# Optimization experiments

Measured on AMD Instinct MI355X. Metric: run time of the kernel, lower is better.

## Reference

```python
import jax, jax.numpy as jnp
import numpy as np

MIN_D, MAX_D = 0.1, 1.0
KSIZE = 5


def gaussian_kernel(ksize):
    sigma = ksize / 6.0
    x = jnp.arange(ksize, dtype=jnp.float32) - ksize // 2
    k1 = jnp.exp(-0.5 * x ** 2 / sigma ** 2)
    k1 = k1 / k1.sum()
    return (k1[:, None] * k1[None, :])[None, None]  # [1,1,k,k]


def setup_inputs() -> dict:
    key = jax.random.key(0)
    k1, k2 = jax.random.split(key)
    B, H, W = 8, 512, 512
    TH = TW = 512
    contrast_map = jax.random.normal(k1, (B, 1, H, W), dtype=jnp.float32)
    # uniform [0,1) randoms replacing the per-sample torch.rand calls
    rand_offsets = jax.random.uniform(k2, (B, TH, TW, 4, 2), dtype=jnp.float32)
    return {
        "contrast_map": contrast_map,
        "rand_offsets": rand_offsets,
        "smoothing_kernel": gaussian_kernel(KSIZE),
        "target_height": TH,
        "target_width": TW,
    }


def reference(contrast_map, rand_offsets, smoothing_kernel, target_height, target_width):
    B, _, H, W = contrast_map.shape
    # per-sample min-max normalization to [0,1]
    mn = contrast_map.min(axis=(1, 2, 3), keepdims=True)
    mx = contrast_map.max(axis=(1, 2, 3), keepdims=True)
    norm = jnp.where(mx > mn, (contrast_map - mn) / (mx - mn), jnp.zeros_like(contrast_map))
    # gaussian smoothing, same padding
    pad = KSIZE // 2
    smoothed = jax.lax.conv_general_dilated(
        norm, smoothing_kernel, window_strides=(1, 1),
        padding=[(pad, pad), (pad, pad)],
        dimension_numbers=("NCHW", "OIHW", "NCHW"))
    # contrast -> density: min_d + (max_d-min_d) * sqrt(c)
    density = MIN_D + (MAX_D - MIN_D) * jnp.sqrt(smoothed)  # [B,1,H,W]

    # nearest-index lookup:  h_idx = floor(i*H/TH) clamped
    hi = jnp.minimum((jnp.arange(target_height) * H) // target_height, H - 1)
    wi = jnp.minimum((jnp.arange(target_width) * W) // target_width, W - 1)
    local = density[:, 0][:, hi][:, :, wi]  # [B,TH,TW]

    # per-pixel sample count: >0.7 -> 4, >0.4 -> 2, else 1
    num_samples = jnp.where(local > 0.7, 4, jnp.where(local > 0.4, 2, 1))  # int [B,TH,TW]

    yb = jnp.linspace(-1.0, 1.0, target_height)
    xb = jnp.linspace(-1.0, 1.0, target_width)
    base = jnp.stack(jnp.broadcast_arrays(yb[:, None], xb[None, :]), axis=-1)  # [TH,TW,2] (y,x)
    cell = jnp.array([2.0 / target_height, 2.0 / target_width], dtype=jnp.float32)
    off = (rand_offsets - 0.5) * cell * 0.8  # [B,TH,TW,4,2]
    use_off = (num_samples > 1)[..., None, None]  # single-sample pixels use the base coord
    coords = base[None, :, :, None, :] + jnp.where(use_off, off, 0.0)  # [B,TH,TW,4,2]

    slot = jnp.arange(4)
    valid = slot[None, None, None, :] < num_samples[..., None]  # [B,TH,TW,4]
    weights = jnp.where(valid, local[..., None] / num_samples[..., None], 0.0)  # [B,TH,TW,4]
    return coords, weights, density
```

## Files before the change

kernel.cpp:

```cpp
#include <hip/hip_runtime.h>

static constexpr int B = 8, Himg = 512, Wimg = 512, TH = 512, TW = 512;
static constexpr int NPIX = B * Himg * Wimg;
static constexpr int BPB = 32;

typedef float f4 __attribute__((ext_vector_type(4)));
typedef float f2 __attribute__((ext_vector_type(2)));

__global__ __launch_bounds__(256) void minmax_kernel(const float* __restrict__ cm,
                                                     float* __restrict__ wsmin,
                                                     float* __restrict__ wsmax) {
    int b   = blockIdx.x / BPB;
    int blk = blockIdx.x % BPB;
    const f4* p = (const f4*)(cm + (size_t)b * Himg * Wimg);
    float mn = 3.4e38f, mx = -3.4e38f;
    int base = blk * 2048;
    #pragma unroll
    for (int k = 0; k < 8; ++k) {
        f4 v = p[base + k * 256 + threadIdx.x];
        mn = fminf(mn, fminf(fminf(v.x, v.y), fminf(v.z, v.w)));
        mx = fmaxf(mx, fmaxf(fmaxf(v.x, v.y), fmaxf(v.z, v.w)));
    }
    #pragma unroll
    for (int off = 32; off; off >>= 1) {
        mn = fminf(mn, __shfl_xor(mn, off));
        mx = fmaxf(mx, __shfl_xor(mx, off));
    }
    __shared__ float smn[4], smx[4];
    int wave = threadIdx.x >> 6, lane = threadIdx.x & 63;
    if (lane == 0) { smn[wave] = mn; smx[wave] = mx; }
    __syncthreads();
    if (threadIdx.x == 0) {
        mn = fminf(fminf(smn[0], smn[1]), fminf(smn[2], smn[3]));
        mx = fmaxf(fmaxf(smx[0], smx[1]), fmaxf(smx[2], smx[3]));
        wsmin[b * BPB + blk] = mn;
        wsmax[b * BPB + blk] = mx;
    }
}

__global__ __launch_bounds__(256) void density_kernel(const float* __restrict__ cm,
                                                      const float* __restrict__ kern,
                                                      const float* __restrict__ wsmin,
                                                      const float* __restrict__ wsmax,
                                                      float* __restrict__ dens) {
    __shared__ double tile[36][37];
    __shared__ double kd[25];
    int tid = threadIdx.x;
    int b = blockIdx.z;
    int bx = blockIdx.x * 32, by = blockIdx.y * 32;
    if (tid < 25) kd[tid] = (double)kern[tid];

    float mnf = 3.4e38f, mxf = -3.4e38f;
    #pragma unroll
    for (int k = 0; k < BPB; ++k) {
        mnf = fminf(mnf, wsmin[b * BPB + k]);
        mxf = fmaxf(mxf, wsmax[b * BPB + k]);
    }
    bool ok = mxf > mnf;
    double mn = (double)mnf;
    double inv = ok ? (1.0 / ((double)mxf - mn)) : 0.0;

    const float* img = cm + (size_t)b * Himg * Wimg;
    for (int idx = tid; idx < 36 * 36; idx += 256) {
        int r = idx / 36, c = idx % 36;
        int gy = by + r - 2, gx = bx + c - 2;
        double v = 0.0;
        if (gy >= 0 && gy < Himg && gx >= 0 && gx < Wimg) {
            double x = (double)img[gy * Wimg + gx];
            v = (x - mn) * inv;
        }
        tile[r][c] = v;
    }
    __syncthreads();

    for (int p = tid; p < 32 * 32; p += 256) {
        int oy = p >> 5, ox = p & 31;
        double s = 0.0;
        #pragma unroll
        for (int dy = 0; dy < 5; ++dy)
            #pragma unroll
            for (int dx = 0; dx < 5; ++dx)
                s += tile[oy + dy][ox + dx] * kd[dy * 5 + dx];
        double D = 0.1 + 0.9 * sqrt(s);
        int code = D > 0.7 ? 2 : (D > 0.4 ? 1 : 0);

        unsigned u = __float_as_uint((float)D);
        u = (u & ~3u) | (unsigned)code;
        dens[(size_t)b * Himg * Wimg + (size_t)(by + oy) * Wimg + (bx + ox)] =
            __uint_as_float(u);
    }
}

__global__ __launch_bounds__(256) void sample_kernel(const float* __restrict__ rnd,
                                                     const float* __restrict__ dens,
                                                     float* __restrict__ coords,
                                                     float* __restrict__ weights) {
    const int stride = 2048 * 256;
    int t0 = blockIdx.x * 256 + threadIdx.x;
    const float cy = (2.0f / TH) * 0.8f;
    const float cx = (2.0f / TW) * 0.8f;

    #pragma unroll
    for (int k = 0; k < 8; ++k) {
        int t = t0 + k * stride;
        int p = t >> 1;
        int h = t & 1;

        float local = dens[p];
        int code = __float_as_uint(local) & 3;
        int num = 1 << code;
        bool useoff = num > 1;

        int rem = p & (Himg * Wimg - 1);
        float yb = -1.0f + (rem >> 9) * (2.0f / (TH - 1));
        float xb = -1.0f + (rem & 511) * (2.0f / (TW - 1));

        f4 r = ((const f4*)rnd)[t];
        f4 c;
        c.x = yb + (useoff ? (r.x - 0.5f) * cy : 0.0f);
        c.y = xb + (useoff ? (r.y - 0.5f) * cx : 0.0f);
        c.z = yb + (useoff ? (r.z - 0.5f) * cy : 0.0f);
        c.w = xb + (useoff ? (r.w - 0.5f) * cx : 0.0f);
        ((f4*)coords)[t] = c;

        float invw = local * __uint_as_float(0x3f800000u - ((unsigned)code << 23));
        f2 w;
        if (h == 0) {
            w.x = invw;
            w.y = (num > 1) ? invw : 0.0f;
        } else {
            float v = (num > 3) ? invw : 0.0f;
            w.x = v;
            w.y = v;
        }
        ((f2*)weights)[t] = w;
    }
}

extern "C" void kernel_launch(void* const* d_in, const int* in_sizes, int n_in,
                              void* d_out, int out_size, void* d_ws, size_t ws_size,
                              hipStream_t stream) {
    const float* cm   = (const float*)d_in[0];
    const float* rnd  = (const float*)d_in[1];
    const float* kern = (const float*)d_in[2];
    float* out     = (float*)d_out;
    float* coords  = out;
    float* weights = out + (size_t)B * TH * TW * 8;
    float* dens    = weights + (size_t)B * TH * TW * 4;
    float* wsmin   = (float*)d_ws;
    float* wsmax   = wsmin + B * BPB;

    minmax_kernel<<<B * BPB, 256, 0, stream>>>(cm, wsmin, wsmax);
    dim3 gridC(Wimg / 32, Himg / 32, B);
    density_kernel<<<gridC, 256, 0, stream>>>(cm, kern, wsmin, wsmax, dens);
    sample_kernel<<<2048, 256, 0, stream>>>(rnd, dens, coords, weights);
}
```

Measured before the change: 50.71 us.

## Fuse density smoothing and sample generation into one tiled kernel

Merges the density and sampling kernels. Each 32x32 tile computes its encoded density into shared memory and then emits coords and weights for those pixels directly. This removes the global re-read of the density map and one kernel launch. The cost is more shared memory per block and a second barrier. The rand/coords accesses become per-row chunks of 512 bytes instead of fully linear streams.

```diff
diff --git a/kernel.cpp b/kernel.cpp
--- a/kernel.cpp
+++ b/kernel.cpp
@@ -1,7 +1,6 @@
 #include <hip/hip_runtime.h>
 
 static constexpr int B = 8, Himg = 512, Wimg = 512, TH = 512, TW = 512;
-static constexpr int NPIX = B * Himg * Wimg;
 static constexpr int BPB = 32;
 
 typedef float f4 __attribute__((ext_vector_type(4)));
@@ -38,16 +37,22 @@
     }
 }
 
-__global__ __launch_bounds__(256) void density_kernel(const float* __restrict__ cm,
-                                                      const float* __restrict__ kern,
-                                                      const float* __restrict__ wsmin,
-                                                      const float* __restrict__ wsmax,
-                                                      float* __restrict__ dens) {
+__global__ __launch_bounds__(256) void fused_kernel(const float* __restrict__ cm,
+                                                    const float* __restrict__ kern,
+                                                    const float* __restrict__ wsmin,
+                                                    const float* __restrict__ wsmax,
+                                                    const float* __restrict__ rnd,
+                                                    float* __restrict__ coords,
+                                                    float* __restrict__ weights,
+                                                    float* __restrict__ dens) {
     __shared__ double tile[36][37];
     __shared__ double kd[25];
+    __shared__ float dsm[1024];
+
     int tid = threadIdx.x;
     int b = blockIdx.z;
     int bx = blockIdx.x * 32, by = blockIdx.y * 32;
+
     if (tid < 25) kd[tid] = (double)kern[tid];
 
     float mnf = 3.4e38f, mxf = -3.4e38f;
@@ -65,10 +70,8 @@
         int r = idx / 36, c = idx % 36;
         int gy = by + r - 2, gx = bx + c - 2;
         double v = 0.0;
-        if (gy >= 0 && gy < Himg && gx >= 0 && gx < Wimg) {
-            double x = (double)img[gy * Wimg + gx];
-            v = (x - mn) * inv;
-        }
+        if (gy >= 0 && gy < Himg && gx >= 0 && gx < Wimg)
+            v = ((double)img[gy * Wimg + gx] - mn) * inv;
         tile[r][c] = v;
     }
     __syncthreads();
@@ -83,45 +86,39 @@
                 s += tile[oy + dy][ox + dx] * kd[dy * 5 + dx];
         double D = 0.1 + 0.9 * sqrt(s);
         int code = D > 0.7 ? 2 : (D > 0.4 ? 1 : 0);
+        unsigned u = (__float_as_uint((float)D) & ~3u) | (unsigned)code;
+        float enc = __uint_as_float(u);
+        dsm[p] = enc;
+        dens[(size_t)b * Himg * Wimg + (size_t)(by + oy) * Wimg + (bx + ox)] = enc;
+    }
+    __syncthreads();
 
-        unsigned u = __float_as_uint((float)D);
-        u = (u & ~3u) | (unsigned)code;
-        dens[(size_t)b * Himg * Wimg + (size_t)(by + oy) * Wimg + (bx + ox)] =
-            __uint_as_float(u);
-    }
-}
-
-__global__ __launch_bounds__(256) void sample_kernel(const float* __restrict__ rnd,
-                                                     const float* __restrict__ dens,
-                                                     float* __restrict__ coords,
-                                                     float* __restrict__ weights) {
-    const int stride = 2048 * 256;
-    int t0 = blockIdx.x * 256 + threadIdx.x;
     const float cy = (2.0f / TH) * 0.8f;
     const float cx = (2.0f / TW) * 0.8f;
-
+    int lane = tid & 63, wv = tid >> 6;
     #pragma unroll
     for (int k = 0; k < 8; ++k) {
-        int t = t0 + k * stride;
-        int p = t >> 1;
-        int h = t & 1;
+        int row = k * 4 + wv;
+        int gy = by + row;
+        int gx = bx + (lane >> 1);
+        int h = lane & 1;
 
-        float local = dens[p];
+        float local = dsm[row * 32 + (lane >> 1)];
         int code = __float_as_uint(local) & 3;
         int num = 1 << code;
         bool useoff = num > 1;
 
-        int rem = p & (Himg * Wimg - 1);
-        float yb = -1.0f + (rem >> 9) * (2.0f / (TH - 1));
-        float xb = -1.0f + (rem & 511) * (2.0f / (TW - 1));
+        float yb = -1.0f + gy * (2.0f / (TH - 1));
+        float xb = -1.0f + gx * (2.0f / (TW - 1));
 
-        f4 r = ((const f4*)rnd)[t];
+        size_t f4i = 2 * ((size_t)b * (Himg * Wimg) + (size_t)gy * Wimg + bx) + lane;
+        f4 r = ((const f4*)rnd)[f4i];
         f4 c;
         c.x = yb + (useoff ? (r.x - 0.5f) * cy : 0.0f);
         c.y = xb + (useoff ? (r.y - 0.5f) * cx : 0.0f);
         c.z = yb + (useoff ? (r.z - 0.5f) * cy : 0.0f);
         c.w = xb + (useoff ? (r.w - 0.5f) * cx : 0.0f);
-        ((f4*)coords)[t] = c;
+        ((f4*)coords)[f4i] = c;
 
         float invw = local * __uint_as_float(0x3f800000u - ((unsigned)code << 23));
         f2 w;
@@ -133,7 +130,7 @@
             w.x = v;
             w.y = v;
         }
-        ((f2*)weights)[t] = w;
+        ((f2*)weights)[f4i] = w;
     }
 }
 
@@ -151,7 +148,7 @@
     float* wsmax   = wsmin + B * BPB;
 
     minmax_kernel<<<B * BPB, 256, 0, stream>>>(cm, wsmin, wsmax);
-    dim3 gridC(Wimg / 32, Himg / 32, B);
-    density_kernel<<<gridC, 256, 0, stream>>>(cm, kern, wsmin, wsmax, dens);
-    sample_kernel<<<2048, 256, 0, stream>>>(rnd, dens, coords, weights);
+    dim3 gridF(Wimg / 32, Himg / 32, B);
+    fused_kernel<<<gridF, 256, 0, stream>>>(cm, kern, wsmin, wsmax, rnd,
+                                            coords, weights, dens);
 }
```

After: 47.54 us (median of 2 runs). -6.3%, faster.
